# Kernel optimization log

Hardware: AMD Instinct MI355X
Metric: run time of the kernel (lower is better)

The kernel has to match this reference:

```python
import jax, jax.numpy as jnp
import numpy as np

IN_F = 4096
OUT_F = 4096
BLOCK_SIZE = 64
BLOCK_NUM = 64
N_FACTOR = 2  # number of butterfly factor matrices (boft_n_butterfly_factor after internal -1, +1)


def block_butterfly_perm(n, b, r, nf):
    # faithful port of BOFTLayer.block_butterfly_perm (static numpy computation)
    if nf == 0:
        return np.arange(n)
    block_size = n // b
    indices = np.arange(n)
    step = block_size / r
    evens = np.arange(0, step, 2)
    odds = np.arange(1, step, 2)
    sorted_seq = np.concatenate([evens, odds]).astype(np.int64)
    sorted_order = np.empty(block_size, dtype=np.int64)
    for i, pos in enumerate(sorted_seq):
        sorted_order[i * r:(i + 1) * r] = np.arange(pos * r, pos * r + r)
    perm = indices.copy()
    for i in range(0, n, block_size):
        perm[i:i + block_size] = indices[i:i + block_size][sorted_order]
    return perm


def _perms():
    return [block_butterfly_perm(IN_F, BLOCK_NUM // (2 ** i), BLOCK_SIZE // 2, N_FACTOR - 1)
            for i in range(N_FACTOR)]


def cayley_batch(R):
    # Q = (I - skew) @ (I + skew)^{-1}, solved as Q (I+skew) = (I-skew)
    skew = 0.5 * (R - jnp.swapaxes(R, -1, -2))
    I = jnp.eye(R.shape[-1], dtype=R.dtype)
    Qt = jnp.linalg.solve(jnp.swapaxes(I + skew, -1, -2), jnp.swapaxes(I - skew, -1, -2))
    return jnp.swapaxes(Qt, -1, -2)


def block_diag_batch(blocks):
    # [D,H,H] -> [D*H, D*H] block-diagonal
    D, H, _ = blocks.shape
    out = jnp.zeros((D * H, D * H), blocks.dtype)
    r = jnp.arange(D)[:, None, None] * H + jnp.arange(H)[None, :, None]
    c = jnp.arange(D)[:, None, None] * H + jnp.arange(H)[None, None, :]
    return out.at[r, c].set(blocks)


def setup_inputs() -> dict:
    key = jax.random.key(0)
    k1, k2, k3, k4 = jax.random.split(key, 4)
    x = jax.random.normal(k1, (2, 2048, IN_F), dtype=jnp.float32)
    weight = jax.random.normal(k2, (OUT_F, IN_F), dtype=jnp.float32) * 0.02
    bias = jax.random.normal(k3, (OUT_F,), dtype=jnp.float32) * 0.02
    boft_R = jax.random.normal(k4, (N_FACTOR, BLOCK_NUM, BLOCK_SIZE, BLOCK_SIZE), dtype=jnp.float32) * 0.1
    boft_s = jnp.ones((OUT_F, 1), dtype=jnp.float32)
    return {"x": x, "weight": weight, "bias": bias, "boft_R": boft_R, "boft_s": boft_s}


def reference(x, weight, bias, boft_R, boft_s):
    N, D, H, _ = boft_R.shape
    Q = cayley_batch(boft_R.reshape(N * D, H, H)).reshape(N, D, H, H)
    perms = _perms()
    rot = jnp.eye(IN_F, dtype=x.dtype)
    for i in range(N):
        B = block_diag_batch(Q[i])                         # [in, in]
        p = perms[i]
        Bp = B[p[:, None], p[None, :]]                     # P @ B @ P^T
        rot = Bp @ rot                                     # compose butterfly factors
    # rotated weight: (rot @ W^T)^T = W @ rot^T, then per-output scaling
    scaled_w = (weight @ rot.T) * boft_s                   # [out, in]
    return x @ scaled_w.T + bias
```

## Files before the change

kernel.cpp:

```cpp
#include <hip/hip_runtime.h>

typedef unsigned short u16;
typedef unsigned int   u32;
typedef __attribute__((ext_vector_type(4))) float f32x4;
typedef __attribute__((ext_vector_type(8))) short bf16x8;
typedef __attribute__((ext_vector_type(4))) unsigned short u16x4;
typedef __attribute__((ext_vector_type(8))) unsigned short u16x8;

__device__ __forceinline__ u16 f2bf(float f) {
  union { float f; u32 u; } v; v.f = f;
  u32 r = v.u + 0x7FFFu + ((v.u >> 16) & 1u);
  return (u16)(r >> 16);
}

__device__ __forceinline__ float bcast(float v, int l) {
  return __uint_as_float(__builtin_amdgcn_readlane(__float_as_uint(v), l));
}

__global__ __launch_bounds__(256, 1) void cayley_kernel(
    const float* __restrict__ R, float* __restrict__ Q) {
  const int b  = blockIdx.x;
  const int t  = threadIdx.x;
  const int j  = t & 63;
  const int iw = t >> 6;
  __shared__ float Rl[64][65];
  __shared__ float prow[2][2][64];
  const float* Rb = R + (size_t)b * 4096;
  for (int idx = t; idx < 4096; idx += 256)
    Rl[idx >> 6][idx & 63] = Rb[idx];
  __syncthreads();
  float Ac[16], Bc[16];
  #pragma unroll
  for (int i2 = 0; i2 < 16; ++i2) {
    const int i = iw*16 + i2;
    float s = 0.5f * (Rl[i][j] - Rl[j][i]);
    Ac[i2] = (i == j) ? (1.0f + s) : s;
    Bc[i2] = (i == j) ? 1.0f : 0.0f;
  }
  __syncthreads();
  #pragma unroll
  for (int kb = 0; kb < 4; ++kb) {
    #pragma unroll
    for (int kp = 0; kp < 16; ++kp) {
      const int k = kb*16 + kp;
      if (iw == kb) {
        float pinv = 1.0f / bcast(Ac[kp], k);
        float ar = Ac[kp] * pinv;
        float br = Bc[kp] * pinv;
        Ac[kp] = ar; Bc[kp] = br;
        prow[k & 1][0][j] = ar;
        prow[k & 1][1][j] = br;
      }
      __syncthreads();
      const float ar = prow[k & 1][0][j];
      const float br = prow[k & 1][1][j];
      #pragma unroll
      for (int i2 = 0; i2 < 16; ++i2) {
        float f = bcast(Ac[i2], k);
        if (iw == kb && i2 == kp) f = 0.0f;
        Ac[i2] -= f * ar;
        Bc[i2] -= f * br;
      }
    }
  }
  float* Qb = Q + (size_t)b * 4096;
  #pragma unroll
  for (int i2 = 0; i2 < 16; ++i2) {
    const int i = iw*16 + i2;
    Qb[i*64 + j] = 2.0f * Bc[i2] - ((i == j) ? 1.0f : 0.0f);
  }
}

__global__ __launch_bounds__(256) void rotbuild_kernel(
    const float* __restrict__ Q, u16* __restrict__ rotb) {
  const int s = blockIdx.x;
  const int t = threadIdx.x;
  __shared__ float Q1l[2][64][65];
  __shared__ f32x4 Q0l[2][64][16];
  const float* Q0g = Q + (size_t)(2*s) * 4096;
  const float* Q1g = Q + (size_t)(64 + 2*s) * 4096;
  for (int i = t; i < 2*4096; i += 256) {
    int e = i >> 12, r = (i >> 6) & 63, c = i & 63;
    Q1l[e][r][c] = Q1g[i];
    ((float*)&Q0l[e][r][0])[c] = Q0g[i];
  }
  __syncthreads();
  const int a_l = t & 127;
  const int dh  = t >> 7;
  const int g   = a_l >> 5;
  const int pa  = a_l + ((g == 1) ? 32 : (g == 2) ? -32 : 0);
  const int e = pa >> 6, pa64 = pa & 63;
  float q1v[32];
  #pragma unroll
  for (int jj = 0; jj < 32; ++jj) q1v[jj] = Q1l[e][pa64][dh*32 + jj];
  f32x4 acc4[16] = {};
  #pragma unroll
  for (int jj = 0; jj < 32; ++jj) {
    #pragma unroll
    for (int c4 = 0; c4 < 16; ++c4)
      acc4[c4] += q1v[jj] * Q0l[dh][e*32 + jj][c4];
  }
  u16* dst = rotb + (size_t)s*16384 + (size_t)a_l*128 + dh*64;
  #pragma unroll
  for (int c4 = 0; c4 < 16; ++c4) {
    u16x4 o;
    o.x = f2bf(acc4[c4].x); o.y = f2bf(acc4[c4].y);
    o.z = f2bf(acc4[c4].z); o.w = f2bf(acc4[c4].w);
    *(u16x4*)&dst[c4*4] = o;
  }
}

__global__ __launch_bounds__(256) void wtrans_kernel(
    const float* __restrict__ W, const u16* __restrict__ rotb,
    const float* __restrict__ sscale, u16* __restrict__ SW) {
  const int rt = blockIdx.x;
  const int s  = blockIdx.y;
  const int t  = threadIdx.x;
  __shared__ u16 Asw[128*128];
  __shared__ u16 Bsw[128*128];
  #pragma unroll
  for (int p = 0; p < 16; ++p) {
    const int g = p*256 + t;
    const int row = g >> 5, gc = g & 31;
    float4 v = *(const float4*)(W + (size_t)(rt*128 + row)*4096 + s*128 + gc*4);
    u16x4 o;
    o.x = f2bf(v.x); o.y = f2bf(v.y); o.z = f2bf(v.z); o.w = f2bf(v.w);
    const int chunk = (gc >> 1) ^ (row & 7);
    *(u16x4*)&Asw[row*128 + chunk*8 + (gc & 1)*4] = o;
  }
  const u16* rsrc = rotb + (size_t)s*16384;
  #pragma unroll
  for (int p = 0; p < 8; ++p) {
    const int g = p*256 + t;
    const int row = g >> 4, ch = g & 15;
    u16x8 v = *(const u16x8*)(rsrc + row*128 + ch*8);
    *(u16x8*)&Bsw[row*128 + ((ch ^ (row & 7))*8)] = v;
  }
  __syncthreads();
  const int w = t >> 6, l = t & 63;
  const int fr = l & 15, fq = l >> 4;
  const int wm = (w >> 1)*64, wn = (w & 1)*64;
  f32x4 acc[4][4] = {};
  #pragma unroll
  for (int ks = 0; ks < 4; ++ks) {
    bf16x8 af[4], bfr[4];
    #pragma unroll
    for (int m = 0; m < 4; ++m)
      af[m] = *(const bf16x8*)&Asw[(wm + m*16 + fr)*128 + (((ks*4 + fq) ^ (fr & 7))*8)];
    #pragma unroll
    for (int n = 0; n < 4; ++n)
      bfr[n] = *(const bf16x8*)&Bsw[(wn + n*16 + fr)*128 + (((ks*4 + fq) ^ (fr & 7))*8)];
    #pragma unroll
    for (int m = 0; m < 4; ++m)
      #pragma unroll
      for (int n = 0; n < 4; ++n)
        acc[m][n] = __builtin_amdgcn_mfma_f32_16x16x32_bf16(
            af[m], bfr[n], acc[m][n], 0, 0, 0);
  }
  #pragma unroll
  for (int m = 0; m < 4; ++m) {
    #pragma unroll
    for (int r = 0; r < 4; ++r) {
      const int row = rt*128 + wm + m*16 + fq*4 + r;
      const float sc = sscale[row];
      #pragma unroll
      for (int n = 0; n < 4; ++n) {
        const int col = s*128 + wn + n*16 + fr;
        SW[(size_t)row*4096 + col] = f2bf(acc[m][n][r] * sc);
      }
    }
  }
}

__global__ __launch_bounds__(256) void cvt_kernel(
    const float* __restrict__ x, u16* __restrict__ xb) {
  const size_t i = (size_t)blockIdx.x * 256 + threadIdx.x;
  const float4* p = (const float4*)x + i*2;
  float4 a = p[0], b = p[1];
  u16x8 o;
  o[0] = f2bf(a.x); o[1] = f2bf(a.y); o[2] = f2bf(a.z); o[3] = f2bf(a.w);
  o[4] = f2bf(b.x); o[5] = f2bf(b.y); o[6] = f2bf(b.z); o[7] = f2bf(b.w);
  *(u16x8*)(xb + i*8) = o;
}

#define GLDS16(g, l)                                                   \
  __builtin_amdgcn_global_load_lds(                                    \
      (const __attribute__((address_space(1))) void*)(g),              \
      (__attribute__((address_space(3))) void*)(l), 16, 0, 0)

__device__ __forceinline__ void bar() {
  asm volatile("" ::: "memory");
  __builtin_amdgcn_s_barrier();
  asm volatile("" ::: "memory");
}

__global__ __launch_bounds__(512, 2) void gemm_kernel(
    const u16* __restrict__ A, const u16* __restrict__ B,
    const float* __restrict__ bias, float* __restrict__ C) {
  constexpr int K = 4096, N = 4096, NT = 64;
  __shared__ u16 As[2*256*64];
  __shared__ u16 Bs[2*256*64];
  const int t = threadIdx.x;
  const int w = t >> 6, l = t & 63;
  const int wr = w >> 2, wc = w & 3;
  const int fr = l & 15, fq = l >> 4;

  const int wg  = blockIdx.x;
  const int swz = (wg & 7) * 32 + (wg >> 3);
  const int m0  = (swz & 15) * 256, n0 = (swz >> 4) * 256;

  const int grow = w*8 + (l >> 3);
  const int gcol = ((l & 7) ^ ((l >> 3) & 7)) * 8;
  const u16* aS = A + (size_t)(m0 + grow) * K + gcol;
  const u16* bS = B + (size_t)(n0 + grow) * K + gcol;
  const int wLds = w * 512;

  const int colbase = (fq ^ (fr & 7)) * 8;
  const u16* aRd = As + (wr*128 + fr)*64;
  const u16* bRd = Bs + (wc*64  + fr)*64;

  auto stgA = [&](int buf, int half, int o, int kt_) {
    GLDS16(aS + (size_t)(half*128 + o*64) * K + (size_t)kt_*64,
           As + buf*16384 + half*8192 + o*4096 + wLds);
  };
  auto stgB = [&](int buf, int half, int o, int kt_) {
    GLDS16(bS + (size_t)(half*128 + o*64) * K + (size_t)kt_*64,
           Bs + buf*16384 + half*8192 + o*4096 + wLds);
  };

  f32x4 acc[8][4] = {};
  bf16x8 aFr[4][2], bFr[4][2];

  stgB(0,0,0,0); stgB(0,0,1,0); stgB(0,1,0,0); stgB(0,1,1,0);
  stgA(0,0,0,0); stgA(0,0,1,0); stgA(0,1,0,0); stgA(0,1,1,0);
  stgB(1,0,0,1); stgB(1,0,1,1); stgB(1,1,0,1); stgB(1,1,1,1);
  stgA(1,0,0,1); stgA(1,0,1,1); stgA(1,1,0,1); stgA(1,1,1,1);
  asm volatile("s_waitcnt vmcnt(8)" ::: "memory");
  bar();

  for (int kt = 0; kt < NT; ++kt) {
    const int cur = kt & 1;
    const u16* aC = aRd + cur*16384;
    const u16* bC = bRd + cur*16384;
    auto lda = [&](int mh) {
      #pragma unroll
      for (int m = 0; m < 4; ++m)
        #pragma unroll
        for (int ks = 0; ks < 2; ++ks)
          aFr[m][ks] = *(const bf16x8*)(aC + (mh*4 + m)*1024 + (colbase ^ (ks << 5)));
    };
    auto ldb = [&](int nh) {
      #pragma unroll
      for (int n = 0; n < 2; ++n)
        #pragma unroll
        for (int ks = 0; ks < 2; ++ks)
          bFr[nh*2 + n][ks] = *(const bf16x8*)(bC + (nh*2 + n)*1024 + (colbase ^ (ks << 5)));
    };
    auto mma = [&](int mh, int nh) {
      __builtin_amdgcn_s_setprio(1);
      #pragma unroll
      for (int m = 0; m < 4; ++m)
        #pragma unroll
        for (int n = 0; n < 2; ++n)
          #pragma unroll
          for (int ks = 0; ks < 2; ++ks)
            acc[mh*4 + m][nh*2 + n] = __builtin_amdgcn_mfma_f32_16x16x32_bf16(
                aFr[m][ks], bFr[nh*2 + n][ks], acc[mh*4 + m][nh*2 + n], 0, 0, 0);
      __builtin_amdgcn_s_setprio(0);
    };
    lda(0); ldb(0);
    bar();
    mma(0, 0);
    bar();
    ldb(1);
    bar();
    mma(0, 1);
    bar();
    if (kt + 2 < NT) { stgB(cur,0,0,kt+2); stgB(cur,0,1,kt+2);
                       stgB(cur,1,0,kt+2); stgB(cur,1,1,kt+2); }
    lda(1);
    bar();
    mma(1, 1);
    bar();
    if (kt + 2 < NT) { stgA(cur,0,0,kt+2); stgA(cur,0,1,kt+2);
                       stgA(cur,1,0,kt+2); stgA(cur,1,1,kt+2); }
    bar();
    mma(1, 0);
    if (kt < NT - 2) {
      asm volatile("s_waitcnt vmcnt(8)" ::: "memory");
    } else if (kt == NT - 2) {
      asm volatile("s_waitcnt vmcnt(0)" ::: "memory");
    }
    bar();
  }

  #pragma unroll
  for (int nf = 0; nf < 4; ++nf) {
    const int col = n0 + wc*64 + nf*16 + fr;
    const float bv = bias[col];
    #pragma unroll
    for (int mf = 0; mf < 8; ++mf) {
      const int rowb = m0 + wr*128 + mf*16 + fq*4;
      #pragma unroll
      for (int r = 0; r < 4; ++r)
        C[(size_t)(rowb + r)*N + col] = acc[mf][nf][r] + bv;
    }
  }
}

extern "C" void kernel_launch(void* const* d_in, const int* in_sizes, int n_in,
                              void* d_out, int out_size, void* d_ws, size_t ws_size,
                              hipStream_t stream) {
  const float* x      = (const float*)d_in[0];
  const float* W      = (const float*)d_in[1];
  const float* bias   = (const float*)d_in[2];
  const float* boft_R = (const float*)d_in[3];
  const float* boft_s = (const float*)d_in[4];
  float* out = (float*)d_out;

  char* ws = (char*)d_ws;
  float* Q    = (float*)ws;
  u16*   rotb = (u16*)  (ws + ((size_t)2  << 20));
  u16*   xb   = (u16*)  (ws + ((size_t)4  << 20));
  u16*   swb  = (u16*)  (ws + ((size_t)36 << 20));

  cayley_kernel  <<<128, 256, 0, stream>>>(boft_R, Q);
  rotbuild_kernel<<<32, 256, 0, stream>>>(Q, rotb);
  wtrans_kernel  <<<dim3(32, 32), 256, 0, stream>>>(W, rotb, boft_s, swb);
  cvt_kernel     <<<(16777216/8)/256, 256, 0, stream>>>(x, xb);
  gemm_kernel    <<<256, 512, 0, stream>>>(xb, swb, bias, out);
}
```

Before: 197.6 us.

## Cut GEMM loop barriers and prefetch next-tile LDS fragments across iterations

The bf16 MFMA main loop is restructured so LDS fragment reads are interleaved with the MFMA groups instead of each being fenced by its own barrier. The first half-fragments of the next k-tile are read at the end of the current iteration. The global-to-LDS wait moves earlier with a tighter vmcnt, so only two barriers per k-step remain. This is meant to remove barrier stalls and hide LDS read latency behind MFMA work. It relies on careful buffer-hazard ordering between the staged loads and the register prefetch.

```diff
diff --git a/kernel.cpp b/kernel.cpp
--- a/kernel.cpp
+++ b/kernel.cpp
@@ -229,7 +229,36 @@
   };
 
   f32x4 acc[8][4] = {};
-  bf16x8 aFr[4][2], bFr[4][2];
+  bf16x8 aF[4][2], bF[4][2];
+
+  auto rdA = [&](int buf, int mh) {
+    const u16* aC = aRd + buf*16384;
+    #pragma unroll
+    for (int m = 0; m < 4; ++m) {
+      aF[m][0] = *(const bf16x8*)(aC + (mh*4 + m)*1024 + colbase);
+      aF[m][1] = *(const bf16x8*)(aC + (mh*4 + m)*1024 + (colbase ^ 32));
+    }
+  };
+  auto rdB = [&](int buf, int nh) {
+    const u16* bC = bRd + buf*16384;
+    #pragma unroll
+    for (int n = 0; n < 2; ++n) {
+      bF[nh*2 + n][0] = *(const bf16x8*)(bC + (nh*2 + n)*1024 + colbase);
+      bF[nh*2 + n][1] = *(const bf16x8*)(bC + (nh*2 + n)*1024 + (colbase ^ 32));
+    }
+  };
+  auto mma = [&](int mh, int nh) {
+    __builtin_amdgcn_s_setprio(1);
+    #pragma unroll
+    for (int m = 0; m < 4; ++m)
+      #pragma unroll
+      for (int n = 0; n < 2; ++n)
+        #pragma unroll
+        for (int ks = 0; ks < 2; ++ks)
+          acc[mh*4 + m][nh*2 + n] = __builtin_amdgcn_mfma_f32_16x16x32_bf16(
+              aF[m][ks], bF[nh*2 + n][ks], acc[mh*4 + m][nh*2 + n], 0, 0, 0);
+    __builtin_amdgcn_s_setprio(0);
+  };
 
   stgB(0,0,0,0); stgB(0,0,1,0); stgB(0,1,0,0); stgB(0,1,1,0);
   stgA(0,0,0,0); stgA(0,0,1,0); stgA(0,1,0,0); stgA(0,1,1,0);
@@ -237,61 +266,28 @@
   stgA(1,0,0,1); stgA(1,0,1,1); stgA(1,1,0,1); stgA(1,1,1,1);
   asm volatile("s_waitcnt vmcnt(8)" ::: "memory");
   bar();
+  rdA(0, 0); rdB(0, 0);
 
   for (int kt = 0; kt < NT; ++kt) {
     const int cur = kt & 1;
-    const u16* aC = aRd + cur*16384;
-    const u16* bC = bRd + cur*16384;
-    auto lda = [&](int mh) {
-      #pragma unroll
-      for (int m = 0; m < 4; ++m)
-        #pragma unroll
-        for (int ks = 0; ks < 2; ++ks)
-          aFr[m][ks] = *(const bf16x8*)(aC + (mh*4 + m)*1024 + (colbase ^ (ks << 5)));
-    };
-    auto ldb = [&](int nh) {
-      #pragma unroll
-      for (int n = 0; n < 2; ++n)
-        #pragma unroll
-        for (int ks = 0; ks < 2; ++ks)
-          bFr[nh*2 + n][ks] = *(const bf16x8*)(bC + (nh*2 + n)*1024 + (colbase ^ (ks << 5)));
-    };
-    auto mma = [&](int mh, int nh) {
-      __builtin_amdgcn_s_setprio(1);
-      #pragma unroll
-      for (int m = 0; m < 4; ++m)
-        #pragma unroll
-        for (int n = 0; n < 2; ++n)
-          #pragma unroll
-          for (int ks = 0; ks < 2; ++ks)
-            acc[mh*4 + m][nh*2 + n] = __builtin_amdgcn_mfma_f32_16x16x32_bf16(
-                aFr[m][ks], bFr[nh*2 + n][ks], acc[mh*4 + m][nh*2 + n], 0, 0, 0);
-      __builtin_amdgcn_s_setprio(0);
-    };
-    lda(0); ldb(0);
-    bar();
     mma(0, 0);
-    bar();
-    ldb(1);
-    bar();
+    rdB(cur, 1);
     mma(0, 1);
+    rdA(cur, 1);
     bar();
     if (kt + 2 < NT) { stgB(cur,0,0,kt+2); stgB(cur,0,1,kt+2);
                        stgB(cur,1,0,kt+2); stgB(cur,1,1,kt+2); }
-    lda(1);
-    bar();
     mma(1, 1);
+    if (kt < NT - 2) {
+      asm volatile("s_waitcnt vmcnt(4)" ::: "memory");
+    } else if (kt == NT - 2) {
+      asm volatile("s_waitcnt vmcnt(0)" ::: "memory");
+    }
     bar();
     if (kt + 2 < NT) { stgA(cur,0,0,kt+2); stgA(cur,0,1,kt+2);
                        stgA(cur,1,0,kt+2); stgA(cur,1,1,kt+2); }
-    bar();
     mma(1, 0);
-    if (kt < NT - 2) {
-      asm volatile("s_waitcnt vmcnt(8)" ::: "memory");
-    } else if (kt == NT - 2) {
-      asm volatile("s_waitcnt vmcnt(0)" ::: "memory");
-    }
-    bar();
+    if (kt + 1 < NT) { rdA(cur ^ 1, 0); rdB(cur ^ 1, 0); }
   }
 
   #pragma unroll
```

Result: faster. 190.3 us (-3.7%).
